# Optimization experiments

Measured on AMD Instinct MI355X. Metric: run time of the kernel, lower is better.

## Reference

```python
import jax, jax.numpy as jnp
import numpy as np
import math

D_MODEL = 2048
N_HEADS = 16
D_K = D_MODEL // N_HEADS


def setup_inputs() -> dict:
    key = jax.random.key(0)
    k0, k1, k2, k3, k4 = jax.random.split(key, 5)
    B, T = 2, 2048
    x = jax.random.normal(k0, (B, T, D_MODEL), dtype=jnp.float32)
    s = 1.0 / math.sqrt(D_MODEL)
    W_qkv = jax.random.normal(k1, (3 * D_MODEL, D_MODEL), dtype=jnp.float32) * s
    b_qkv = jax.random.normal(k2, (3 * D_MODEL,), dtype=jnp.float32) * 0.01
    W_out = jax.random.normal(k3, (D_MODEL, D_MODEL), dtype=jnp.float32) * s
    b_out = jax.random.normal(k4, (D_MODEL,), dtype=jnp.float32) * 0.01
    return {"x": x, "W_qkv": W_qkv, "b_qkv": b_qkv, "W_out": W_out, "b_out": b_out}


def reference(x, W_qkv, b_qkv, W_out, b_out):
    B, T, C = x.shape
    qkv = x @ W_qkv.T + b_qkv                      # [B,T,3C]
    q, k, v = jnp.split(qkv, 3, axis=-1)
    # [B,T,C] -> [B,H,T,Dk]
    def to_heads(t):
        return t.reshape(B, T, N_HEADS, D_K).transpose(0, 2, 1, 3)
    q, k, v = to_heads(q), to_heads(k), to_heads(v)
    scale = 1.0 / math.sqrt(D_K)
    scores = jnp.einsum('bhqd,bhkd->bhqk', q, k) * scale   # [B,H,T,T]
    causal = jnp.tril(jnp.ones((T, T), dtype=bool))
    neg = jnp.finfo(scores.dtype).min
    scores = jnp.where(causal[None, None], scores, neg)
    attn = jax.nn.softmax(scores, axis=-1)
    out = jnp.einsum('bhqk,bhkd->bhqd', attn, v)           # [B,H,T,Dk]
    out = out.transpose(0, 2, 1, 3).reshape(B, T, C)
    return out @ W_out.T + b_out
```

## Files before the change

kernel.cpp:

```cpp
#include <hip/hip_runtime.h>
#include <stdint.h>

typedef short bf16x8 __attribute__((ext_vector_type(8)));
typedef float f32x4 __attribute__((ext_vector_type(4)));
typedef float f32x16 __attribute__((ext_vector_type(16)));
typedef unsigned short u16;
typedef unsigned int u32;

__device__ __forceinline__ u16 f2bf(float f) {
    u32 x = __float_as_uint(f);
    x += 0x7fffu + ((x >> 16) & 1u);
    return (u16)(x >> 16);
}
__device__ __forceinline__ u32 pack_bf2(float a, float b) {
    return (u32)f2bf(a) | ((u32)f2bf(b) << 16);
}
__device__ __forceinline__ float bf2f(u16 v) {
    return __uint_as_float(((u32)v) << 16);
}

union Frag4 { u32 u[4]; bf16x8 v; };

__device__ __forceinline__ void gload16(const u16* g, u16* l) {
    __builtin_amdgcn_global_load_lds(
        (__attribute__((address_space(1))) void*)g,
        (__attribute__((address_space(3))) void*)l,
        16, 0, 0);
}

__global__ void cvt_f32_bf16(const float* __restrict__ in, u16* __restrict__ out, long n8) {
    long stride = (long)gridDim.x * blockDim.x;
    for (long i = (long)blockIdx.x * blockDim.x + threadIdx.x; i < n8; i += stride) {
        const float4* p = (const float4*)(in + i * 8);
        float4 a = p[0], b = p[1];
        uint4 o;
        o.x = pack_bf2(a.x, a.y);
        o.y = pack_bf2(a.z, a.w);
        o.z = pack_bf2(b.x, b.y);
        o.w = pack_bf2(b.z, b.w);
        ((uint4*)out)[i] = o;
    }
}

template<int OBF>
__global__ __launch_bounds__(256, 2) void gemm_nt(
    const u16* __restrict__ A, const u16* __restrict__ B,
    const float* __restrict__ bias, void* __restrict__ out,
    int K, int ldo, int gxsh)
{
    __shared__ __align__(16) u16 lA[2 * 128 * 64];
    __shared__ __align__(16) u16 lB[2 * 128 * 64];
    const int tid  = threadIdx.x;
    const int lane = tid & 63;
    const int w    = tid >> 6;
    const int wm = (w >> 1) * 64, wn = (w & 1) * 64;

    const int nwg = gridDim.x;
    const int bid = blockIdx.x;
    const int swz = (bid & 7) * (nwg >> 3) + (bid >> 3);
    const int bm = (swz & ((1 << gxsh) - 1)) * 128;
    const int bn = (swz >> gxsh) * 128;

    const int lr = lane >> 3;
    const u32 sb = (u32)((lane & 7) * 16);
    const int NT = K >> 6;

    auto stage = [&](int bb, int k0) {
#pragma unroll
        for (int i = 0; i < 4; ++i) {
            const int c = w * 4 + i;
            const int row = c * 8 + lr;
            const u32 col = (sb ^ ((u32)(row & 7) << 4)) >> 1;
            gload16(A + (size_t)(bm + row) * K + k0 + col, lA + bb * 8192 + c * 512);
            gload16(B + (size_t)(bn + row) * K + k0 + col, lB + bb * 8192 + c * 512);
        }
    };

    f32x4 acc[4][4];
#pragma unroll
    for (int i = 0; i < 4; ++i)
#pragma unroll
        for (int j = 0; j < 4; ++j)
#pragma unroll
            for (int r = 0; r < 4; ++r) acc[i][j][r] = 0.f;

    stage(0, 0);
    stage(1, 64);
    asm volatile("s_waitcnt vmcnt(8)" ::: "memory");
    __builtin_amdgcn_sched_barrier(0);
    __builtin_amdgcn_s_barrier();
    __builtin_amdgcn_sched_barrier(0);

    for (int t = 0; t < NT; ++t) {
        const int cur = t & 1;
        const char* pA = (const char*)(lA + cur * 8192);
        const char* pB = (const char*)(lB + cur * 8192);
#pragma unroll
        for (int kk = 0; kk < 2; ++kk) {
            bf16x8 af[4], bfr[4];
#pragma unroll
            for (int f = 0; f < 4; ++f) {
                const int m = wm + f * 16 + (lane & 15);
                const u32 byt = (u32)(kk * 64 + (lane >> 4) * 16) ^ ((u32)(m & 7) << 4);
                af[f]  = *(const bf16x8*)(pA + m * 128 + byt);
                const int n = wn + f * 16 + (lane & 15);
                const u32 bytb = (u32)(kk * 64 + (lane >> 4) * 16) ^ ((u32)(n & 7) << 4);
                bfr[f] = *(const bf16x8*)(pB + n * 128 + bytb);
            }
            __builtin_amdgcn_s_setprio(1);
#pragma unroll
            for (int i = 0; i < 4; ++i)
#pragma unroll
                for (int j = 0; j < 4; ++j)
                    acc[i][j] = __builtin_amdgcn_mfma_f32_16x16x32_bf16(af[i], bfr[j], acc[i][j], 0, 0, 0);
            __builtin_amdgcn_s_setprio(0);
        }
        __builtin_amdgcn_sched_barrier(0);
        __builtin_amdgcn_s_barrier();
        __builtin_amdgcn_sched_barrier(0);
        if (t + 2 < NT) {
            stage(cur, (t + 2) * 64);
            asm volatile("s_waitcnt vmcnt(8)" ::: "memory");
        } else {
            asm volatile("s_waitcnt vmcnt(0)" ::: "memory");
        }
        __builtin_amdgcn_sched_barrier(0);
        __builtin_amdgcn_s_barrier();
        __builtin_amdgcn_sched_barrier(0);
    }

#pragma unroll
    for (int i = 0; i < 4; ++i) {
        int m0 = bm + wm + i * 16 + ((lane >> 4) << 2);
#pragma unroll
        for (int j = 0; j < 4; ++j) {
            int n = bn + wn + j * 16 + (lane & 15);
            float bv = bias[n];
#pragma unroll
            for (int r = 0; r < 4; ++r) {
                float v = acc[i][j][r] + bv;
                if constexpr (OBF != 0)
                    ((u16*)out)[(size_t)(m0 + r) * ldo + n] = f2bf(v);
                else
                    ((float*)out)[(size_t)(m0 + r) * ldo + n] = v;
            }
        }
    }
}

__global__ __launch_bounds__(256) void transpose_v(
    const u16* __restrict__ qkv, u16* __restrict__ vt)
{
    __shared__ u16 lt[64 * 64];
    const int tid = threadIdx.x;
    const int bid = blockIdx.x;
    const int tt    = bid & 31;
    const int dtile = (bid >> 5) & 1;
    const int h     = (bid >> 6) & 15;
    const int b     = bid >> 10;
    const u16* src = qkv + ((size_t)b * 2048 + tt * 64) * 6144 + 4096 + h * 128 + dtile * 64;

    const int r = tid >> 2, ce = (tid & 3) * 16;
    uint4 a0 = *(const uint4*)(src + (size_t)r * 6144 + ce);
    uint4 a1 = *(const uint4*)(src + (size_t)r * 6144 + ce + 8);
    const u32 swz = (u32)((r & 7) << 4);
    *(uint4*)((char*)lt + r * 128 + (((u32)(ce * 2)) ^ swz)) = a0;
    *(uint4*)((char*)lt + r * 128 + (((u32)(ce * 2 + 16)) ^ swz)) = a1;
    __syncthreads();

    const int d = tid >> 2;
    u16* dst = vt + ((size_t)(b * 16 + h) * 128 + dtile * 64 + d) * 2048 + tt * 64;
#pragma unroll
    for (int it = 0; it < 2; ++it) {
        const int t0 = (tid & 3) * 8 + it * 32;
        union { u16 hh[8]; uint4 q4; } u;
#pragma unroll
        for (int uu = 0; uu < 8; ++uu) {
            int trow = t0 + uu;
            u32 byt = (u32)(trow * 128) + (((u32)(d * 2)) ^ ((u32)((trow & 7) << 4)));
            u.hh[uu] = *(const u16*)((const char*)lt + byt);
        }
        *(uint4*)(dst + t0) = u.q4;
    }
}

__constant__ unsigned char QT_TAB[30] = {11,11, 5,15,15,15,10,10,14,14,14, 9, 9, 4,13,13,13,12,12,12, 8, 8, 7, 7, 3, 6, 6, 2, 1, 0};
__constant__ unsigned char TLO_TAB[30]= { 0,24, 0, 0,22,43, 0,22, 0,20,40, 0,20, 0, 0,19,38, 0,18,36, 0,18, 0,16, 0, 0,14, 0, 0, 0};
__constant__ unsigned char THI_TAB[30]= {24,48,24,22,43,64,22,44,20,40,60,20,40,20,19,38,56,18,36,52,18,36,16,32,16,14,28,12, 8, 4};
__constant__ unsigned char SL_TAB[30] = {10,11,255,21,22,23, 8, 9,18,19,20, 6, 7,255,15,16,17,12,13,14, 4, 5, 2, 3,255, 0, 1,255,255,255};

__global__ __launch_bounds__(256) void attn_fwd(
    const u16* __restrict__ qkv, const u16* __restrict__ vt,
    u16* __restrict__ obuf, u16* __restrict__ pout, float* __restrict__ pml)
{
    __shared__ __align__(16) u16 lS[17408];
    const int tid  = threadIdx.x;
    const int lane = tid & 63;
    const int w    = tid >> 6;
    const int g    = lane >> 5;
    const int ql   = lane & 31;

    const int bid  = blockIdx.x;
    const int item = bid >> 5;
    const int bh   = bid & 31;
    const int qt   = QT_TAB[item];
    const int slot = SL_TAB[item];
    const int t_lo = TLO_TAB[item];
    const int t_hi = THI_TAB[item];
    const int b = bh >> 4, h = bh & 15;
    const size_t rowbase = (size_t)b * 2048;
    const int qb = qt * 128;
    const int qw = qb + w * 32;
    const int q  = qw + ql;

    const u16* Khead = qkv + rowbase * 6144 + 2048 + h * 128;
    const u16* Vth   = vt + (size_t)bh * 128 * 2048;

    bf16x8 qf[8];
    {
        const u16* qrow = qkv + (rowbase + q) * 6144 + h * 128;
#pragma unroll
        for (int ch = 0; ch < 8; ++ch)
            qf[ch] = *(const bf16x8*)(qrow + ch * 16 + g * 8);
    }

    f32x16 acc[4];
#pragma unroll
    for (int dt = 0; dt < 4; ++dt)
#pragma unroll
        for (int r = 0; r < 16; ++r) acc[dt][r] = 0.f;

    float m_run = -1e30f, l_run = 0.f;
    const float C2 = 0.08838834764831845f * 1.44269504088896341f;

    auto stage = [&](int bb, int t) {
        const int kb = t * 32;
#pragma unroll
        for (int i = 0; i < 2; ++i) {
            const int c = w * 2 + i;
            const int kr = c * 4 + (lane >> 4);
            const u32 kcol = (((u32)((lane & 15) * 16)) ^ ((u32)(kr & 7) << 4)) >> 1;
            gload16(Khead + (size_t)(kb + kr) * 6144 + kcol,
                    lS + bb * 4096 + c * 512);
            const int vr = c * 16 + (lane >> 2);
            const u32 vcol = (((u32)((lane & 3) * 16)) ^ ((u32)(vr & 3) << 4)) >> 1;
            gload16(Vth + (size_t)vr * 2048 + kb + vcol,
                    lS + 8192 + bb * 4096 + c * 512);
        }
    };

    stage(0, t_lo);
    __syncthreads();
    int buf = 0;

    for (int t = t_lo; t < t_hi; ++t) {
        const int kb = t * 32;
        if (t + 1 < t_hi) stage(buf ^ 1, t + 1);

        if (kb <= qw + 31) {
            const char* lKb = (const char*)(lS + buf * 4096);
            const char* lVb = (const char*)(lS + 8192 + buf * 4096);
            const bool diag = (kb == qw);

            bf16x8 kf[8];
            const u32 ksw = ((u32)ql & 7) << 4;
#pragma unroll
            for (int ch = 0; ch < 8; ++ch)
                kf[ch] = *(const bf16x8*)(lKb + ql * 256 + (((u32)(ch * 32 + g * 16)) ^ ksw));

            f32x16 s_;
#pragma unroll
            for (int r = 0; r < 16; ++r) s_[r] = 0.f;
            __builtin_amdgcn_s_setprio(1);
#pragma unroll
            for (int ch = 0; ch < 8; ++ch)
                s_ = __builtin_amdgcn_mfma_f32_32x32x16_bf16(kf[ch], qf[ch], s_, 0, 0, 0);
            __builtin_amdgcn_s_setprio(0);

            float p[16];
            float tmax = -1e30f;
#pragma unroll
            for (int r = 0; r < 16; ++r) {
                int crow = (r & 3) + 8 * (r >> 2) + 4 * g;
                float v = s_[r];
                if (diag && (crow > ql)) v = -1e30f;
                p[r] = v;
                tmax = fmaxf(tmax, v);
            }
            tmax = fmaxf(tmax, __shfl_xor(tmax, 32));
            if (!__all(tmax <= m_run + 8.0f)) {
                float mnew  = fmaxf(m_run, tmax);
                float alpha = exp2f((m_run - mnew) * C2);
#pragma unroll
                for (int dt = 0; dt < 4; ++dt) acc[dt] = acc[dt] * alpha;
                l_run *= alpha;
                m_run = mnew;
            }
            float ssum = 0.f;
#pragma unroll
            for (int r = 0; r < 16; ++r) {
                float e = exp2f((p[r] - m_run) * C2);
                p[r] = e;
                ssum += e;
            }
            ssum += __shfl_xor(ssum, 32);
            l_run += ssum;

            u32 wb[8], sw[8];
#pragma unroll
            for (int j = 0; j < 8; ++j) wb[j] = pack_bf2(p[2 * j], p[2 * j + 1]);
#pragma unroll
            for (int j = 0; j < 8; ++j) sw[j] = __shfl_xor(wb[j], 32);
            Frag4 pf0, pf1;
#pragma unroll
            for (int u = 0; u < 4; ++u) {
                const bool own = (g == (u >> 1));
                pf0.u[u] = own ? wb[2 * g + (u & 1)]     : sw[2 * g + (u & 1)];
                pf1.u[u] = own ? wb[4 + 2 * g + (u & 1)] : sw[4 + 2 * g + (u & 1)];
            }

            __builtin_amdgcn_s_setprio(1);
#pragma unroll
            for (int dt = 0; dt < 4; ++dt) {
                const u32 vrow = (u32)(dt * 32 + ql);
                const u32 vsw = (vrow & 3) << 4;
                bf16x8 v0 = *(const bf16x8*)(lVb + vrow * 64 + (((u32)(g * 16)) ^ vsw));
                bf16x8 v1 = *(const bf16x8*)(lVb + vrow * 64 + (((u32)(32 + g * 16)) ^ vsw));
                acc[dt] = __builtin_amdgcn_mfma_f32_32x32x16_bf16(v0, pf0.v, acc[dt], 0, 0, 0);
                acc[dt] = __builtin_amdgcn_mfma_f32_32x32x16_bf16(v1, pf1.v, acc[dt], 0, 0, 0);
            }
            __builtin_amdgcn_s_setprio(0);
        }
        __syncthreads();
        buf ^= 1;
    }

    const float scale = (slot == 255) ? (1.0f / l_run) : 1.0f;
    u16* lO = lS + w * 4352;
#pragma unroll
    for (int dt = 0; dt < 4; ++dt) {
#pragma unroll
        for (int rr = 0; rr < 4; ++rr) {
            int d0 = dt * 32 + rr * 8 + g * 4;
            int r0 = rr * 4;
            u32* dst = (u32*)(lO + ql * 136 + d0);
            dst[0] = pack_bf2(acc[dt][r0] * scale,     acc[dt][r0 + 1] * scale);
            dst[1] = pack_bf2(acc[dt][r0 + 2] * scale, acc[dt][r0 + 3] * scale);
        }
    }
    if (slot != 255 && g == 0) {
        const int sg = bh * 24 + slot;
        float2* pm = (float2*)pml + sg * 128 + (w * 32 + ql);
        *pm = make_float2(m_run, l_run);
    }
    __syncthreads();

    u16* gbase;
    size_t rstride;
    if (slot == 255) {
        gbase = obuf + (rowbase + qw) * 2048 + h * 128;
        rstride = 2048;
    } else {
        const int sg = bh * 24 + slot;
        gbase = pout + (size_t)sg * 16384 + (size_t)(w * 32) * 128;
        rstride = 128;
    }
    const int eo = (lane & 15) * 8;
#pragma unroll
    for (int pass = 0; pass < 8; ++pass) {
        const int row = pass * 4 + (lane >> 4);
        bf16x8 v = *(const bf16x8*)(lO + row * 136 + eo);
        *(bf16x8*)(gbase + (size_t)row * rstride + eo) = v;
    }
}

__global__ __launch_bounds__(256) void attn_merge(
    const u16* __restrict__ pout, const float* __restrict__ pml,
    u16* __restrict__ obuf)
{
    const int bid = blockIdx.x;
    const int bh = bid & 31, j = bid >> 5;
    const int qt = 6 + j;
    const int b = bh >> 4, h = bh & 15;
    const int tid = threadIdx.x;
    const int f  = (qt < 12) ? 2 : 3;
    const int sb = (qt < 12) ? (qt - 6) * 2 : 12 + (qt - 12) * 3;
    const int base = bh * 24 + sb;
    const float C2 = 0.08838834764831845f * 1.44269504088896341f;
    const int eo = (tid & 15) * 8;

#pragma unroll
    for (int pass = 0; pass < 8; ++pass) {
        const int row = pass * 16 + (tid >> 4);
        float mv[3], lv[3], wv[3];
        float ms = -1e30f;
#pragma unroll
        for (int i = 0; i < 3; ++i) {
            if (i < f) {
                float2 ml = ((const float2*)pml)[(base + i) * 128 + row];
                mv[i] = ml.x; lv[i] = ml.y;
                ms = fmaxf(ms, ml.x);
            }
        }
        float L = 0.f;
#pragma unroll
        for (int i = 0; i < 3; ++i) {
            if (i < f) {
                wv[i] = exp2f((mv[i] - ms) * C2);
                L += lv[i] * wv[i];
            }
        }
        const float inv = 1.0f / L;

        float o[8];
#pragma unroll
        for (int e = 0; e < 8; ++e) o[e] = 0.f;
#pragma unroll
        for (int i = 0; i < 3; ++i) {
            if (i < f) {
                bf16x8 v = *(const bf16x8*)(pout + (size_t)(base + i) * 16384
                                            + (size_t)row * 128 + eo);
#pragma unroll
                for (int e = 0; e < 8; ++e) o[e] += wv[i] * bf2f((u16)v[e]);
            }
        }
        u16* orow = obuf + ((size_t)b * 2048 + qt * 128 + row) * 2048 + h * 128 + eo;
#pragma unroll
        for (int e = 0; e < 8; e += 2)
            *(u32*)(orow + e) = pack_bf2(o[e] * inv, o[e + 1] * inv);
    }
}

extern "C" void kernel_launch(void* const* d_in, const int* in_sizes, int n_in,
                              void* d_out, int out_size, void* d_ws, size_t ws_size,
                              hipStream_t stream) {
    (void)in_sizes; (void)n_in; (void)out_size; (void)ws_size;
    const float* x    = (const float*)d_in[0];
    const float* Wqkv = (const float*)d_in[1];
    const float* bqkv = (const float*)d_in[2];
    const float* Wout = (const float*)d_in[3];
    const float* bout = (const float*)d_in[4];

    char* ws = (char*)d_ws;
    u16* xb  = (u16*)ws;
    u16* wqb = (u16*)(ws + (size_t)16777216);
    u16* qkv = (u16*)(ws + (size_t)41943040);
    u16* ob  = xb;
    u16* vtb = wqb;
    u16* wob = wqb;
    float* pml = (float*)(ws + (size_t)33554432);
    u16* pO  = (u16*)d_out;

    cvt_f32_bf16<<<2048, 256, 0, stream>>>(x, xb, 8388608L / 8);
    cvt_f32_bf16<<<2048, 256, 0, stream>>>(Wqkv, wqb, 12582912L / 8);
    gemm_nt<1><<<1536, 256, 0, stream>>>(xb, wqb, bqkv, qkv, 2048, 6144, 5);
    transpose_v<<<2048, 256, 0, stream>>>(qkv, vtb);
    attn_fwd<<<960, 256, 0, stream>>>(qkv, vtb, ob, pO, pml);
    attn_merge<<<320, 256, 0, stream>>>(pO, pml, ob);
    cvt_f32_bf16<<<2048, 256, 0, stream>>>(Wout, wob, 4194304L / 8);
    gemm_nt<0><<<512, 256, 0, stream>>>(ob, wob, bout, d_out, 2048, 2048, 5);
}
```

Before: 299.0 us.

## Use 256x256 tile GEMM with 512 threads for QKV projection

```diff
diff --git a/kernel.cpp b/kernel.cpp
--- a/kernel.cpp
+++ b/kernel.cpp
@@ -39,6 +39,110 @@
         o.z = pack_bf2(b.x, b.y);
         o.w = pack_bf2(b.z, b.w);
         ((uint4*)out)[i] = o;
+    }
+}
+
+__global__ __launch_bounds__(512, 2) void gemm256_nt(
+    const u16* __restrict__ A, const u16* __restrict__ B,
+    const float* __restrict__ bias, u16* __restrict__ out,
+    int K, int ldo, int gxsh)
+{
+    __shared__ __align__(16) u16 lA[2 * 256 * 64];
+    __shared__ __align__(16) u16 lB[2 * 256 * 64];
+    const int tid  = threadIdx.x;
+    const int lane = tid & 63;
+    const int w    = tid >> 6;
+    const int wm = (w >> 2) * 128;
+    const int wn = (w & 3) * 64;
+
+    const int nwg = gridDim.x;
+    const int bid = blockIdx.x;
+    const int swz = (bid & 7) * (nwg >> 3) + (bid >> 3);
+    const int bm = (swz & ((1 << gxsh) - 1)) * 256;
+    const int bn = (swz >> gxsh) * 256;
+
+    const int lr = lane >> 3;
+    const u32 sb = (u32)((lane & 7) * 16);
+    const int NT = K >> 6;
+
+    auto stage = [&](int bb, int k0) {
+#pragma unroll
+        for (int i = 0; i < 4; ++i) {
+            const int c = w * 4 + i;
+            const int row = c * 8 + lr;
+            const u32 col = (sb ^ ((u32)(row & 7) << 4)) >> 1;
+            gload16(A + (size_t)(bm + row) * K + k0 + col, lA + bb * 16384 + c * 512);
+            gload16(B + (size_t)(bn + row) * K + k0 + col, lB + bb * 16384 + c * 512);
+        }
+    };
+
+    f32x4 acc[8][4];
+#pragma unroll
+    for (int i = 0; i < 8; ++i)
+#pragma unroll
+        for (int j = 0; j < 4; ++j)
+#pragma unroll
+            for (int r = 0; r < 4; ++r) acc[i][j][r] = 0.f;
+
+    stage(0, 0);
+    stage(1, 64);
+    asm volatile("s_waitcnt vmcnt(8)" ::: "memory");
+    __builtin_amdgcn_sched_barrier(0);
+    __builtin_amdgcn_s_barrier();
+    __builtin_amdgcn_sched_barrier(0);
+
+    for (int t = 0; t < NT; ++t) {
+        const int cur = t & 1;
+        const char* pA = (const char*)(lA + cur * 16384);
+        const char* pB = (const char*)(lB + cur * 16384);
+#pragma unroll
+        for (int kk = 0; kk < 2; ++kk) {
+            bf16x8 af[8], bfr[4];
+#pragma unroll
+            for (int f = 0; f < 8; ++f) {
+                const int m = wm + f * 16 + (lane & 15);
+                const u32 byt = (u32)(kk * 64 + (lane >> 4) * 16) ^ ((u32)(m & 7) << 4);
+                af[f] = *(const bf16x8*)(pA + m * 128 + byt);
+            }
+#pragma unroll
+            for (int j = 0; j < 4; ++j) {
+                const int n = wn + j * 16 + (lane & 15);
+                const u32 byt = (u32)(kk * 64 + (lane >> 4) * 16) ^ ((u32)(n & 7) << 4);
+                bfr[j] = *(const bf16x8*)(pB + n * 128 + byt);
+            }
+            __builtin_amdgcn_s_setprio(1);
+#pragma unroll
+            for (int i = 0; i < 8; ++i)
+#pragma unroll
+                for (int j = 0; j < 4; ++j)
+                    acc[i][j] = __builtin_amdgcn_mfma_f32_16x16x32_bf16(af[i], bfr[j], acc[i][j], 0, 0, 0);
+            __builtin_amdgcn_s_setprio(0);
+        }
+        __builtin_amdgcn_sched_barrier(0);
+        __builtin_amdgcn_s_barrier();
+        __builtin_amdgcn_sched_barrier(0);
+        if (t + 2 < NT) {
+            stage(cur, (t + 2) * 64);
+            asm volatile("s_waitcnt vmcnt(8)" ::: "memory");
+        } else {
+            asm volatile("s_waitcnt vmcnt(0)" ::: "memory");
+        }
+        __builtin_amdgcn_sched_barrier(0);
+        __builtin_amdgcn_s_barrier();
+        __builtin_amdgcn_sched_barrier(0);
+    }
+
+#pragma unroll
+    for (int i = 0; i < 8; ++i) {
+        int m0 = bm + wm + i * 16 + ((lane >> 4) << 2);
+#pragma unroll
+        for (int j = 0; j < 4; ++j) {
+            int n = bn + wn + j * 16 + (lane & 15);
+            float bv = bias[n];
+#pragma unroll
+            for (int r = 0; r < 4; ++r)
+                out[(size_t)(m0 + r) * ldo + n] = f2bf(acc[i][j][r] + bv);
+        }
     }
 }
 
@@ -453,7 +557,7 @@
 
     cvt_f32_bf16<<<2048, 256, 0, stream>>>(x, xb, 8388608L / 8);
     cvt_f32_bf16<<<2048, 256, 0, stream>>>(Wqkv, wqb, 12582912L / 8);
-    gemm_nt<1><<<1536, 256, 0, stream>>>(xb, wqb, bqkv, qkv, 2048, 6144, 5);
+    gemm256_nt<<<384, 512, 0, stream>>>(xb, wqb, bqkv, qkv, 2048, 6144, 4);
     transpose_v<<<2048, 256, 0, stream>>>(qkv, vtb);
     attn_fwd<<<960, 256, 0, stream>>>(qkv, vtb, ob, pO, pml);
     attn_merge<<<320, 256, 0, stream>>>(pO, pml, ob);
```

Result: slower. 321.3 us (+7.5%).

## Use 8-wave 128x128 GEMM blocks and fuse the two input conversions

Applied to the files above, without the earlier changes.

```diff
diff --git a/kernel.cpp b/kernel.cpp
--- a/kernel.cpp
+++ b/kernel.cpp
@@ -42,8 +42,28 @@
     }
 }
 
+__global__ void cvt2_f32_bf16(const float* __restrict__ inA, u16* __restrict__ outA, long n8A,
+                              const float* __restrict__ inB, u16* __restrict__ outB, long n8B) {
+    long stride = (long)gridDim.x * blockDim.x;
+    const long tot = n8A + n8B;
+    for (long i = (long)blockIdx.x * blockDim.x + threadIdx.x; i < tot; i += stride) {
+        const float4* p;
+        uint4* q;
+        if (i < n8A) { p = (const float4*)(inA + i * 8);        q = (uint4*)outA + i; }
+        else         { long j = i - n8A;
+                       p = (const float4*)(inB + j * 8);        q = (uint4*)outB + j; }
+        float4 a = p[0], b = p[1];
+        uint4 o;
+        o.x = pack_bf2(a.x, a.y);
+        o.y = pack_bf2(a.z, a.w);
+        o.z = pack_bf2(b.x, b.y);
+        o.w = pack_bf2(b.z, b.w);
+        *q = o;
+    }
+}
+
 template<int OBF>
-__global__ __launch_bounds__(256, 2) void gemm_nt(
+__global__ __launch_bounds__(512, 2) void gemm128_8w(
     const u16* __restrict__ A, const u16* __restrict__ B,
     const float* __restrict__ bias, void* __restrict__ out,
     int K, int ldo, int gxsh)
@@ -53,7 +73,8 @@
     const int tid  = threadIdx.x;
     const int lane = tid & 63;
     const int w    = tid >> 6;
-    const int wm = (w >> 1) * 64, wn = (w & 1) * 64;
+    const int wm = (w >> 2) * 64;
+    const int wn = (w & 3) * 32;
 
     const int nwg = gridDim.x;
     const int bid = blockIdx.x;
@@ -67,8 +88,8 @@
 
     auto stage = [&](int bb, int k0) {
 #pragma unroll
-        for (int i = 0; i < 4; ++i) {
-            const int c = w * 4 + i;
+        for (int i = 0; i < 2; ++i) {
+            const int c = w * 2 + i;
             const int row = c * 8 + lr;
             const u32 col = (sb ^ ((u32)(row & 7) << 4)) >> 1;
             gload16(A + (size_t)(bm + row) * K + k0 + col, lA + bb * 8192 + c * 512);
@@ -76,17 +97,17 @@
         }
     };
 
-    f32x4 acc[4][4];
+    f32x4 acc[4][2];
 #pragma unroll
     for (int i = 0; i < 4; ++i)
 #pragma unroll
-        for (int j = 0; j < 4; ++j)
+        for (int j = 0; j < 2; ++j)
 #pragma unroll
             for (int r = 0; r < 4; ++r) acc[i][j][r] = 0.f;
 
     stage(0, 0);
     stage(1, 64);
-    asm volatile("s_waitcnt vmcnt(8)" ::: "memory");
+    asm volatile("s_waitcnt vmcnt(4)" ::: "memory");
     __builtin_amdgcn_sched_barrier(0);
     __builtin_amdgcn_s_barrier();
     __builtin_amdgcn_sched_barrier(0);
@@ -97,21 +118,24 @@
         const char* pB = (const char*)(lB + cur * 8192);
 #pragma unroll
         for (int kk = 0; kk < 2; ++kk) {
-            bf16x8 af[4], bfr[4];
+            bf16x8 af[4], bfr[2];
 #pragma unroll
             for (int f = 0; f < 4; ++f) {
                 const int m = wm + f * 16 + (lane & 15);
                 const u32 byt = (u32)(kk * 64 + (lane >> 4) * 16) ^ ((u32)(m & 7) << 4);
-                af[f]  = *(const bf16x8*)(pA + m * 128 + byt);
-                const int n = wn + f * 16 + (lane & 15);
-                const u32 bytb = (u32)(kk * 64 + (lane >> 4) * 16) ^ ((u32)(n & 7) << 4);
-                bfr[f] = *(const bf16x8*)(pB + n * 128 + bytb);
+                af[f] = *(const bf16x8*)(pA + m * 128 + byt);
+            }
+#pragma unroll
+            for (int j = 0; j < 2; ++j) {
+                const int n = wn + j * 16 + (lane & 15);
+                const u32 byt = (u32)(kk * 64 + (lane >> 4) * 16) ^ ((u32)(n & 7) << 4);
+                bfr[j] = *(const bf16x8*)(pB + n * 128 + byt);
             }
             __builtin_amdgcn_s_setprio(1);
 #pragma unroll
             for (int i = 0; i < 4; ++i)
 #pragma unroll
-                for (int j = 0; j < 4; ++j)
+                for (int j = 0; j < 2; ++j)
                     acc[i][j] = __builtin_amdgcn_mfma_f32_16x16x32_bf16(af[i], bfr[j], acc[i][j], 0, 0, 0);
             __builtin_amdgcn_s_setprio(0);
         }
@@ -120,7 +144,7 @@
         __builtin_amdgcn_sched_barrier(0);
         if (t + 2 < NT) {
             stage(cur, (t + 2) * 64);
-            asm volatile("s_waitcnt vmcnt(8)" ::: "memory");
+            asm volatile("s_waitcnt vmcnt(4)" ::: "memory");
         } else {
             asm volatile("s_waitcnt vmcnt(0)" ::: "memory");
         }
@@ -133,7 +157,7 @@
     for (int i = 0; i < 4; ++i) {
         int m0 = bm + wm + i * 16 + ((lane >> 4) << 2);
 #pragma unroll
-        for (int j = 0; j < 4; ++j) {
+        for (int j = 0; j < 2; ++j) {
             int n = bn + wn + j * 16 + (lane & 15);
             float bv = bias[n];
 #pragma unroll
@@ -451,12 +475,12 @@
     float* pml = (float*)(ws + (size_t)33554432);
     u16* pO  = (u16*)d_out;
 
-    cvt_f32_bf16<<<2048, 256, 0, stream>>>(x, xb, 8388608L / 8);
-    cvt_f32_bf16<<<2048, 256, 0, stream>>>(Wqkv, wqb, 12582912L / 8);
-    gemm_nt<1><<<1536, 256, 0, stream>>>(xb, wqb, bqkv, qkv, 2048, 6144, 5);
+    cvt2_f32_bf16<<<2048, 256, 0, stream>>>(x, xb, 8388608L / 8,
+                                            Wqkv, wqb, 12582912L / 8);
+    gemm128_8w<1><<<1536, 512, 0, stream>>>(xb, wqb, bqkv, qkv, 2048, 6144, 5);
     transpose_v<<<2048, 256, 0, stream>>>(qkv, vtb);
     attn_fwd<<<960, 256, 0, stream>>>(qkv, vtb, ob, pO, pml);
     attn_merge<<<320, 256, 0, stream>>>(pO, pml, ob);
     cvt_f32_bf16<<<2048, 256, 0, stream>>>(Wout, wob, 4194304L / 8);
-    gemm_nt<0><<<512, 256, 0, stream>>>(ob, wob, bout, d_out, 2048, 2048, 5);
-}
+    gemm128_8w<0><<<512, 512, 0, stream>>>(ob, wob, bout, d_out, 2048, 2048, 5);
+}
```

Measured after the change: 298.3 us. About the same (-0.2%).
